# Kernel optimization log

Measured on AMD Instinct MI355X. Metric: run time of the kernel, lower is better.

Reference implementation:

```python
import jax, jax.numpy as jnp
import numpy as np

VOCAB, HIDDEN, NUM_LABELS = 400000, 300, 7
B, S = 256, 512


def setup_inputs() -> dict:
    key = jax.random.key(0)
    ks = jax.random.split(key, 8)
    return {
        "input_ids": jax.random.randint(ks[0], (B, S), 0, VOCAB, dtype=jnp.int64 if jax.config.jax_enable_x64 else jnp.int32).astype(jnp.int32),
        "attention_masks": jax.random.randint(ks[1], (B, S), 0, 2).astype(jnp.int32),
        "labels": jax.random.randint(ks[2], (B,), 0, NUM_LABELS).astype(jnp.int32),
        "drop_mask": jax.random.randint(ks[3], (B, S), 0, 2).astype(jnp.int32),
        "emb_table": jax.random.normal(ks[4], (VOCAB, HIDDEN), dtype=jnp.float32) * 0.1,
        "W1": jax.random.normal(ks[5], (HIDDEN, HIDDEN), dtype=jnp.float32) * 0.05,
        "b1": jnp.zeros((HIDDEN,), jnp.float32),
        "W2": jax.random.normal(ks[6], (HIDDEN, HIDDEN), dtype=jnp.float32) * 0.05,
        "b2": jnp.zeros((HIDDEN,), jnp.float32),
        "W3": jax.random.normal(ks[7], (NUM_LABELS, HIDDEN), dtype=jnp.float32) * 0.05,
        "b3": jnp.zeros((NUM_LABELS,), jnp.float32),
    }


def reference(input_ids, attention_masks, labels, drop_mask, emb_table, W1, b1, W2, b2, W3, b3):
    # masked token ids (padding -> id 0), then embedding gather: [B,S,H]
    masked = input_ids * attention_masks
    embs = emb_table[masked]
    # NOTE: original's per-element torch.mul loop discards results, so the
    # dropout mask only affects the divisor via count_nonzero per row.
    nonzeros = jnp.sum(drop_mask, axis=1).astype(jnp.float32)  # [B]
    avg = jnp.sum(embs, axis=1) / nonzeros[:, None]            # [B,H]
    h = jax.nn.relu(avg @ W1.T + b1)
    h = jax.nn.relu(h @ W2.T + b2)
    logits = h @ W3.T + b3                                     # [B,7]
    logp = jax.nn.log_softmax(logits, axis=-1)
    loss = -jnp.mean(jnp.take_along_axis(logp, labels[:, None], axis=1))
    return loss, logits
```

## Files before the change

kernel.cpp:

```cpp
#include <hip/hip_runtime.h>
#include <hip/hip_bf16.h>

#define B_ 256
#define S_ 512
#define H_ 300
#define NL_ 7
#define NT_ 320
#define NCHUNK_ 4
#define SPER_ (S_ / NCHUNK_)

__global__ __launch_bounds__(NT_) void dan_gather(
    const int* __restrict__ ids, const int* __restrict__ am,
    const float* __restrict__ emb, float* __restrict__ partial) {
  const int b = blockIdx.x, c = blockIdx.y, t = threadIdx.x;
  __shared__ int sid[SPER_];
  const int s0 = c * SPER_;
  for (int s = t; s < SPER_; s += NT_) {
    int off = b * S_ + s0 + s;
    sid[s] = ids[off] * am[off];
  }
  __syncthreads();
  if (t < H_) {
    const float* ep = emb + t;
    float a0 = 0.f, a1 = 0.f, a2 = 0.f, a3 = 0.f;
#pragma unroll 4
    for (int s = 0; s < SPER_; s += 4) {
      int i0 = sid[s], i1 = sid[s + 1], i2 = sid[s + 2], i3 = sid[s + 3];
      a0 += ep[(size_t)i0 * H_];
      a1 += ep[(size_t)i1 * H_];
      a2 += ep[(size_t)i2 * H_];
      a3 += ep[(size_t)i3 * H_];
    }
    partial[(b * NCHUNK_ + c) * H_ + t] = (a0 + a1) + (a2 + a3);
  }
}

__global__ __launch_bounds__(NT_) void dan_mlp(
    const float* __restrict__ partial, const int* __restrict__ drop,
    const int* __restrict__ labels,
    const float* __restrict__ W1, const float* __restrict__ b1,
    const float* __restrict__ W2, const float* __restrict__ b2,
    const float* __restrict__ W3, const float* __restrict__ b3,
    float* __restrict__ out, float* __restrict__ perloss) {
  const int b = blockIdx.x, t = threadIdx.x;
  __shared__ float savg[H_];
  __shared__ float sh[H_];
  __shared__ float swred[NT_ / 64];
  __shared__ float snz;
  __shared__ float slog[NL_];

  int nzp = 0;
  for (int s = t; s < S_; s += NT_) nzp += drop[b * S_ + s];
  for (int o = 32; o > 0; o >>= 1) nzp += __shfl_down(nzp, o, 64);
  if ((t & 63) == 0) swred[t >> 6] = (float)nzp;
  __syncthreads();
  if (t == 0) {
    float s = 0.f;
    for (int w = 0; w < NT_ / 64; ++w) s += swred[w];
    snz = s;
  }
  __syncthreads();

  if (t < H_) {
    float s = 0.f;
#pragma unroll
    for (int c = 0; c < NCHUNK_; ++c) s += partial[(b * NCHUNK_ + c) * H_ + t];
    savg[t] = s / snz;
  }
  __syncthreads();

  if (t < H_) {
    float acc = b1[t];
    const float* w = W1 + t * H_;
    for (int j = 0; j < H_; ++j) acc = fmaf(w[j], savg[j], acc);
    sh[t] = fmaxf(acc, 0.f);
  }
  __syncthreads();

  if (t < H_) {
    float acc = b2[t];
    const float* w = W2 + t * H_;
    for (int j = 0; j < H_; ++j) acc = fmaf(w[j], sh[j], acc);
    savg[t] = fmaxf(acc, 0.f);
  }
  __syncthreads();

  if (t < NL_) {
    float acc = b3[t];
    const float* w = W3 + t * H_;
    for (int j = 0; j < H_; ++j) acc = fmaf(w[j], savg[j], acc);
    slog[t] = acc;
    out[1 + b * NL_ + t] = acc;
  }
  __syncthreads();

  if (t == 0) {
    float m = slog[0];
    for (int c = 1; c < NL_; ++c) m = fmaxf(m, slog[c]);
    float se = 0.f;
    for (int c = 0; c < NL_; ++c) se += expf(slog[c] - m);
    int lab = labels[b];
    perloss[b] = slog[lab] - m - logf(se);
  }
}

__global__ void dan_loss(const float* __restrict__ perloss,
                         float* __restrict__ out) {
  const int t = threadIdx.x;
  float v = perloss[t];
  for (int o = 32; o > 0; o >>= 1) v += __shfl_down(v, o, 64);
  __shared__ float r[4];
  if ((t & 63) == 0) r[t >> 6] = v;
  __syncthreads();
  if (t == 0) out[0] = -(r[0] + r[1] + r[2] + r[3]) * (1.0f / B_);
}

extern "C" void kernel_launch(void* const* d_in, const int* in_sizes, int n_in,
                              void* d_out, int out_size, void* d_ws,
                              size_t ws_size, hipStream_t stream) {
  const int* ids = (const int*)d_in[0];
  const int* am = (const int*)d_in[1];
  const int* labels = (const int*)d_in[2];
  const int* drop = (const int*)d_in[3];
  const float* emb = (const float*)d_in[4];
  const float* W1 = (const float*)d_in[5];
  const float* b1 = (const float*)d_in[6];
  const float* W2 = (const float*)d_in[7];
  const float* b2 = (const float*)d_in[8];
  const float* W3 = (const float*)d_in[9];
  const float* b3 = (const float*)d_in[10];
  float* out = (float*)d_out;

  float* partial = (float*)d_ws;
  float* perloss = partial + (size_t)B_ * NCHUNK_ * H_;

  dan_gather<<<dim3(B_, NCHUNK_), NT_, 0, stream>>>(ids, am, emb, partial);
  dan_mlp<<<B_, NT_, 0, stream>>>(partial, drop, labels, W1, b1, W2, b2, W3,
                                  b3, out, perloss);
  dan_loss<<<1, B_, 0, stream>>>(perloss, out);
}
```

Measured before the change: 46.43 us.

## Compact nonzero token ids before gather and pre-transpose MLP weights

The gather kernel now compacts the nonzero masked ids with a ballot and popcount, so padded tokens (id 0) are not gathered individually. It adds a single (count of padded tokens) * emb[0] term per column to keep the sum exact. The same launch also runs extra blocks that transpose W1 and W2 into workspace, so the MLP's per-thread dot products read weights coalesced across threads instead of striding by row. The cost is extra workspace, extra shared-memory bookkeeping, and a small reordering of float sums.

```diff
diff --git a/kernel.cpp b/kernel.cpp
--- a/kernel.cpp
+++ b/kernel.cpp
@@ -9,37 +9,86 @@
 #define NCHUNK_ 4
 #define SPER_ (S_ / NCHUNK_)
 
-__global__ __launch_bounds__(NT_) void dan_gather(
+#define NGATHER_ (B_ * NCHUNK_)
+#define NTILE_ 10
+#define NTRANS_ (2 * NTILE_ * NTILE_)
+
+__global__ __launch_bounds__(NT_) void dan_gather_t(
     const int* __restrict__ ids, const int* __restrict__ am,
-    const float* __restrict__ emb, float* __restrict__ partial) {
-  const int b = blockIdx.x, c = blockIdx.y, t = threadIdx.x;
-  __shared__ int sid[SPER_];
-  const int s0 = c * SPER_;
-  for (int s = t; s < SPER_; s += NT_) {
-    int off = b * S_ + s0 + s;
-    sid[s] = ids[off] * am[off];
-  }
-  __syncthreads();
-  if (t < H_) {
-    const float* ep = emb + t;
-    float a0 = 0.f, a1 = 0.f, a2 = 0.f, a3 = 0.f;
-#pragma unroll 4
-    for (int s = 0; s < SPER_; s += 4) {
-      int i0 = sid[s], i1 = sid[s + 1], i2 = sid[s + 2], i3 = sid[s + 3];
-      a0 += ep[(size_t)i0 * H_];
-      a1 += ep[(size_t)i1 * H_];
-      a2 += ep[(size_t)i2 * H_];
-      a3 += ep[(size_t)i3 * H_];
+    const float* __restrict__ emb,
+    const float* __restrict__ W1, const float* __restrict__ W2,
+    float* __restrict__ partial, float* __restrict__ WT1,
+    float* __restrict__ WT2) {
+  const int bid = blockIdx.x;
+  const int t = threadIdx.x;
+
+  if (bid < NGATHER_) {
+    const int b = bid >> 2, c = bid & 3;
+    __shared__ int cid[SPER_ + 8];
+    __shared__ int wcnt[2];
+    __shared__ int snnzp;
+
+    int id = 0;
+    if (t < SPER_) {
+      int off = b * S_ + c * SPER_ + t;
+      id = ids[off] * am[off];
     }
-    partial[(b * NCHUNK_ + c) * H_ + t] = (a0 + a1) + (a2 + a3);
+    for (int s = t; s < SPER_ + 8; s += NT_) cid[s] = 0;
+    unsigned long long m = __ballot(id != 0);
+    const int lane = t & 63;
+    if (t < SPER_ && lane == 0) wcnt[t >> 6] = __popcll(m);
+    __syncthreads();
+    if (t < SPER_ && id != 0) {
+      int base = (t >> 6) ? wcnt[0] : 0;
+      int rank = __popcll(m & ((1ull << lane) - 1));
+      cid[base + rank] = id;
+    }
+    if (t == 0) snnzp = (wcnt[0] + wcnt[1] + 7) & ~7;
+    __syncthreads();
+
+    if (t < H_) {
+      const float* ep = emb + t;
+      const int nnzp = snnzp;
+      float a0 = 0.f, a1 = 0.f, a2 = 0.f, a3 = 0.f;
+#pragma unroll 2
+      for (int s = 0; s < nnzp; s += 8) {
+        a0 += ep[(size_t)cid[s] * H_];
+        a1 += ep[(size_t)cid[s + 1] * H_];
+        a2 += ep[(size_t)cid[s + 2] * H_];
+        a3 += ep[(size_t)cid[s + 3] * H_];
+        a0 += ep[(size_t)cid[s + 4] * H_];
+        a1 += ep[(size_t)cid[s + 5] * H_];
+        a2 += ep[(size_t)cid[s + 6] * H_];
+        a3 += ep[(size_t)cid[s + 7] * H_];
+      }
+      float r = (a0 + a1) + (a2 + a3) + (float)(SPER_ - nnzp) * ep[0];
+      partial[bid * H_ + t] = r;
+    }
+  } else {
+    int tid = bid - NGATHER_;
+    const float* src = (tid < NTILE_ * NTILE_) ? W1 : W2;
+    float* dst = (tid < NTILE_ * NTILE_) ? WT1 : WT2;
+    int tile = (tid < NTILE_ * NTILE_) ? tid : tid - NTILE_ * NTILE_;
+    int by = (tile / NTILE_) * 32, bx = (tile % NTILE_) * 32;
+    __shared__ float stile[32][33];
+    int tx = t & 31, ty = t >> 5;
+    for (int r = ty; r < 32; r += 10) {
+      int row = by + r, col = bx + tx;
+      if (row < H_ && col < H_) stile[r][tx] = src[row * H_ + col];
+    }
+    __syncthreads();
+    for (int r = ty; r < 32; r += 10) {
+      int row = bx + r, col = by + tx;
+      if (row < H_ && col < H_) dst[row * H_ + col] = stile[tx][r];
+    }
   }
 }
 
 __global__ __launch_bounds__(NT_) void dan_mlp(
     const float* __restrict__ partial, const int* __restrict__ drop,
     const int* __restrict__ labels,
-    const float* __restrict__ W1, const float* __restrict__ b1,
-    const float* __restrict__ W2, const float* __restrict__ b2,
+    const float* __restrict__ WT1, const float* __restrict__ b1,
+    const float* __restrict__ WT2, const float* __restrict__ b2,
     const float* __restrict__ W3, const float* __restrict__ b3,
     float* __restrict__ out, float* __restrict__ perloss) {
   const int b = blockIdx.x, t = threadIdx.x;
@@ -71,16 +120,18 @@
 
   if (t < H_) {
     float acc = b1[t];
-    const float* w = W1 + t * H_;
-    for (int j = 0; j < H_; ++j) acc = fmaf(w[j], savg[j], acc);
+    const float* w = WT1 + t;
+#pragma unroll 10
+    for (int j = 0; j < H_; ++j) acc = fmaf(w[(size_t)j * H_], savg[j], acc);
     sh[t] = fmaxf(acc, 0.f);
   }
   __syncthreads();
 
   if (t < H_) {
     float acc = b2[t];
-    const float* w = W2 + t * H_;
-    for (int j = 0; j < H_; ++j) acc = fmaf(w[j], sh[j], acc);
+    const float* w = WT2 + t;
+#pragma unroll 10
+    for (int j = 0; j < H_; ++j) acc = fmaf(w[(size_t)j * H_], sh[j], acc);
     savg[t] = fmaxf(acc, 0.f);
   }
   __syncthreads();
@@ -132,10 +183,13 @@
   float* out = (float*)d_out;
 
   float* partial = (float*)d_ws;
-  float* perloss = partial + (size_t)B_ * NCHUNK_ * H_;
+  float* perloss = partial + (size_t)NGATHER_ * H_;
+  float* WT1 = perloss + B_;
+  float* WT2 = WT1 + (size_t)H_ * H_;
 
-  dan_gather<<<dim3(B_, NCHUNK_), NT_, 0, stream>>>(ids, am, emb, partial);
-  dan_mlp<<<B_, NT_, 0, stream>>>(partial, drop, labels, W1, b1, W2, b2, W3,
+  dan_gather_t<<<NGATHER_ + NTRANS_, NT_, 0, stream>>>(ids, am, emb, W1, W2,
+                                                       partial, WT1, WT2);
+  dan_mlp<<<B_, NT_, 0, stream>>>(partial, drop, labels, WT1, b1, WT2, b2, W3,
                                   b3, out, perloss);
   dan_loss<<<1, B_, 0, stream>>>(perloss, out);
 }
```

Result: slower. 50.77 us (+9.3%).

## Fuse gather, MLP and loss into one kernel with last-block reduction

Applied to the files above, without the earlier changes.

Merges the three kernels into a single 640-thread block per batch row. Two thread groups split the sequence for the embedding gather, and the dense layers become wave-per-row dot products with shuffle reductions. The final loss mean is computed by the last block to finish, detected with an atomic counter that is cleared by a memset. This removes two launches and the global partial-sum round trip, but the gather now uses only 256 blocks instead of 1024, which lowers the memory-level parallelism available to it.

```diff
diff --git a/kernel.cpp b/kernel.cpp
--- a/kernel.cpp
+++ b/kernel.cpp
@@ -5,92 +5,108 @@
 #define S_ 512
 #define H_ 300
 #define NL_ 7
-#define NT_ 320
-#define NCHUNK_ 4
-#define SPER_ (S_ / NCHUNK_)
+#define NT_ 640
+#define GRP_ 320
+#define NWAVE_ 10
 
-__global__ __launch_bounds__(NT_) void dan_gather(
+__global__ __launch_bounds__(NT_) void dan_fused(
     const int* __restrict__ ids, const int* __restrict__ am,
-    const float* __restrict__ emb, float* __restrict__ partial) {
-  const int b = blockIdx.x, c = blockIdx.y, t = threadIdx.x;
-  __shared__ int sid[SPER_];
-  const int s0 = c * SPER_;
-  for (int s = t; s < SPER_; s += NT_) {
-    int off = b * S_ + s0 + s;
-    sid[s] = ids[off] * am[off];
-  }
-  __syncthreads();
-  if (t < H_) {
-    const float* ep = emb + t;
-    float a0 = 0.f, a1 = 0.f, a2 = 0.f, a3 = 0.f;
-#pragma unroll 4
-    for (int s = 0; s < SPER_; s += 4) {
-      int i0 = sid[s], i1 = sid[s + 1], i2 = sid[s + 2], i3 = sid[s + 3];
-      a0 += ep[(size_t)i0 * H_];
-      a1 += ep[(size_t)i1 * H_];
-      a2 += ep[(size_t)i2 * H_];
-      a3 += ep[(size_t)i3 * H_];
-    }
-    partial[(b * NCHUNK_ + c) * H_ + t] = (a0 + a1) + (a2 + a3);
-  }
-}
-
-__global__ __launch_bounds__(NT_) void dan_mlp(
-    const float* __restrict__ partial, const int* __restrict__ drop,
-    const int* __restrict__ labels,
+    const int* __restrict__ labels, const int* __restrict__ drop,
+    const float* __restrict__ emb,
     const float* __restrict__ W1, const float* __restrict__ b1,
     const float* __restrict__ W2, const float* __restrict__ b2,
     const float* __restrict__ W3, const float* __restrict__ b3,
-    float* __restrict__ out, float* __restrict__ perloss) {
+    float* __restrict__ out, float* __restrict__ perloss,
+    unsigned* __restrict__ cnt) {
   const int b = blockIdx.x, t = threadIdx.x;
+  __shared__ int sid[S_];
+  __shared__ float sred[H_];
   __shared__ float savg[H_];
-  __shared__ float sh[H_];
-  __shared__ float swred[NT_ / 64];
+  __shared__ float sh1[H_];
+  __shared__ float sh2[H_];
+  __shared__ float swred[8];
   __shared__ float snz;
   __shared__ float slog[NL_];
 
-  int nzp = 0;
-  for (int s = t; s < S_; s += NT_) nzp += drop[b * S_ + s];
-  for (int o = 32; o > 0; o >>= 1) nzp += __shfl_down(nzp, o, 64);
-  if ((t & 63) == 0) swred[t >> 6] = (float)nzp;
+  if (t < S_) {
+    int off = b * S_ + t;
+    sid[t] = ids[off] * am[off];
+    int dv = drop[off];
+    for (int o = 32; o > 0; o >>= 1) dv += __shfl_down(dv, o, 64);
+    if ((t & 63) == 0) swred[t >> 6] = (float)dv;
+  }
   __syncthreads();
   if (t == 0) {
-    float s = 0.f;
-    for (int w = 0; w < NT_ / 64; ++w) s += swred[w];
-    snz = s;
+    float s2 = 0.f;
+    for (int w = 0; w < 8; ++w) s2 += swred[w];
+    snz = s2;
   }
   __syncthreads();
 
-  if (t < H_) {
-    float s = 0.f;
-#pragma unroll
-    for (int c = 0; c < NCHUNK_; ++c) s += partial[(b * NCHUNK_ + c) * H_ + t];
-    savg[t] = s / snz;
+  const int g = (t >= GRP_) ? 1 : 0;
+  const int lt = t - g * GRP_;
+  float a0 = 0.f, a1 = 0.f, a2 = 0.f, a3 = 0.f;
+  if (lt < H_) {
+    const float* ep = emb + lt;
+    const int s0 = g * (S_ / 2);
+#pragma unroll 2
+    for (int s = s0; s < s0 + S_ / 2; s += 8) {
+      a0 += ep[sid[s] * H_];
+      a1 += ep[sid[s + 1] * H_];
+      a2 += ep[sid[s + 2] * H_];
+      a3 += ep[sid[s + 3] * H_];
+      a0 += ep[sid[s + 4] * H_];
+      a1 += ep[sid[s + 5] * H_];
+      a2 += ep[sid[s + 6] * H_];
+      a3 += ep[sid[s + 7] * H_];
+    }
+  }
+  if (g == 1 && lt < H_) sred[lt] = (a0 + a1) + (a2 + a3);
+  __syncthreads();
+  if (g == 0 && lt < H_)
+    savg[lt] = ((a0 + a1) + (a2 + a3) + sred[lt]) / snz;
+  __syncthreads();
+
+  const int wv = t >> 6;
+  const int lane = t & 63;
+
+  for (int i = wv; i < H_; i += NWAVE_) {
+    const float* row = W1 + i * H_;
+    float d = row[lane] * savg[lane];
+    d = fmaf(row[lane + 64], savg[lane + 64], d);
+    d = fmaf(row[lane + 128], savg[lane + 128], d);
+    d = fmaf(row[lane + 192], savg[lane + 192], d);
+    if (lane < H_ - 256) d = fmaf(row[lane + 256], savg[lane + 256], d);
+    for (int o = 32; o > 0; o >>= 1) d += __shfl_xor(d, o, 64);
+    if (lane == 0) sh1[i] = fmaxf(d + b1[i], 0.f);
   }
   __syncthreads();
 
-  if (t < H_) {
-    float acc = b1[t];
-    const float* w = W1 + t * H_;
-    for (int j = 0; j < H_; ++j) acc = fmaf(w[j], savg[j], acc);
-    sh[t] = fmaxf(acc, 0.f);
+  for (int i = wv; i < H_; i += NWAVE_) {
+    const float* row = W2 + i * H_;
+    float d = row[lane] * sh1[lane];
+    d = fmaf(row[lane + 64], sh1[lane + 64], d);
+    d = fmaf(row[lane + 128], sh1[lane + 128], d);
+    d = fmaf(row[lane + 192], sh1[lane + 192], d);
+    if (lane < H_ - 256) d = fmaf(row[lane + 256], sh1[lane + 256], d);
+    for (int o = 32; o > 0; o >>= 1) d += __shfl_xor(d, o, 64);
+    if (lane == 0) sh2[i] = fmaxf(d + b2[i], 0.f);
   }
   __syncthreads();
 
-  if (t < H_) {
-    float acc = b2[t];
-    const float* w = W2 + t * H_;
-    for (int j = 0; j < H_; ++j) acc = fmaf(w[j], sh[j], acc);
-    savg[t] = fmaxf(acc, 0.f);
-  }
-  __syncthreads();
-
-  if (t < NL_) {
-    float acc = b3[t];
-    const float* w = W3 + t * H_;
-    for (int j = 0; j < H_; ++j) acc = fmaf(w[j], savg[j], acc);
-    slog[t] = acc;
-    out[1 + b * NL_ + t] = acc;
+  if (wv < NL_) {
+    const float* row = W3 + wv * H_;
+    float d = row[lane] * sh2[lane];
+    d = fmaf(row[lane + 64], sh2[lane + 64], d);
+    d = fmaf(row[lane + 128], sh2[lane + 128], d);
+    d = fmaf(row[lane + 192], sh2[lane + 192], d);
+    if (lane < H_ - 256) d = fmaf(row[lane + 256], sh2[lane + 256], d);
+    for (int o = 32; o > 0; o >>= 1) d += __shfl_xor(d, o, 64);
+    if (lane == 0) {
+      d += b3[wv];
+      slog[wv] = d;
+      out[1 + b * NL_ + wv] = d;
+    }
   }
   __syncthreads();
 
@@ -102,17 +118,23 @@
     int lab = labels[b];
     perloss[b] = slog[lab] - m - logf(se);
   }
-}
+  __syncthreads();
 
-__global__ void dan_loss(const float* __restrict__ perloss,
-                         float* __restrict__ out) {
-  const int t = threadIdx.x;
-  float v = perloss[t];
-  for (int o = 32; o > 0; o >>= 1) v += __shfl_down(v, o, 64);
-  __shared__ float r[4];
-  if ((t & 63) == 0) r[t >> 6] = v;
-  __syncthreads();
-  if (t == 0) out[0] = -(r[0] + r[1] + r[2] + r[3]) * (1.0f / B_);
+  if (t < 64) {
+    unsigned old = 0;
+    if (t == 0) {
+      __threadfence();
+      old = atomicAdd(cnt, 1u);
+    }
+    old = __shfl(old, 0, 64);
+    if (old == B_ - 1) {
+      __threadfence();
+      float v = perloss[t] + perloss[t + 64] + perloss[t + 128] +
+                perloss[t + 192];
+      for (int o = 32; o > 0; o >>= 1) v += __shfl_xor(v, o, 64);
+      if (t == 0) out[0] = -v * (1.0f / (float)B_);
+    }
+  }
 }
 
 extern "C" void kernel_launch(void* const* d_in, const int* in_sizes, int n_in,
@@ -131,11 +153,10 @@
   const float* b3 = (const float*)d_in[10];
   float* out = (float*)d_out;
 
-  float* partial = (float*)d_ws;
-  float* perloss = partial + (size_t)B_ * NCHUNK_ * H_;
+  float* perloss = (float*)d_ws;
+  unsigned* cnt = (unsigned*)((char*)d_ws + B_ * sizeof(float));
 
-  dan_gather<<<dim3(B_, NCHUNK_), NT_, 0, stream>>>(ids, am, emb, partial);
-  dan_mlp<<<B_, NT_, 0, stream>>>(partial, drop, labels, W1, b1, W2, b2, W3,
-                                  b3, out, perloss);
-  dan_loss<<<1, B_, 0, stream>>>(perloss, out);
+  hipMemsetAsync(cnt, 0, sizeof(unsigned), stream);
+  dan_fused<<<B_, NT_, 0, stream>>>(ids, am, labels, drop, emb, W1, b1, W2,
+                                    b2, W3, b3, out, perloss, cnt);
 }
```

After: 74.84 us. 1.61x slower.

## Vectorize embedding gather with float4 rows split across token groups

Applied to the files above, without the earlier changes.

The gather kernel now has each thread load float4 slices of an embedding row, and the 300 threads are split into four token groups of 75 threads each. The four group partial sums are combined through shared memory. The MLP matvecs also switch to float4 loads of the weights and activations. The aim is fewer, wider memory transactions per gathered row, at the cost of an extra shared-memory reduction and barrier, and strided float4 weight reads per thread.

```diff
diff --git a/kernel.cpp b/kernel.cpp
--- a/kernel.cpp
+++ b/kernel.cpp
@@ -8,31 +8,49 @@
 #define NT_ 320
 #define NCHUNK_ 4
 #define SPER_ (S_ / NCHUNK_)
+#define NGATHER_ (B_ * NCHUNK_)
+
+#define Q_ (H_ / 4)
+
+__device__ __forceinline__ void f4add(float4& a, const float4 b) {
+  a.x += b.x; a.y += b.y; a.z += b.z; a.w += b.w;
+}
 
 __global__ __launch_bounds__(NT_) void dan_gather(
     const int* __restrict__ ids, const int* __restrict__ am,
     const float* __restrict__ emb, float* __restrict__ partial) {
-  const int b = blockIdx.x, c = blockIdx.y, t = threadIdx.x;
+  const int gb = blockIdx.x;
+  const int b = gb >> 2, c = gb & 3;
+  const int t = threadIdx.x;
   __shared__ int sid[SPER_];
-  const int s0 = c * SPER_;
-  for (int s = t; s < SPER_; s += NT_) {
-    int off = b * S_ + s0 + s;
-    sid[s] = ids[off] * am[off];
+  __shared__ __align__(16) float sacc[4][H_];
+
+  if (t < SPER_) {
+    int off = b * S_ + c * SPER_ + t;
+    sid[t] = ids[off] * am[off];
   }
   __syncthreads();
+
   if (t < H_) {
-    const float* ep = emb + t;
-    float a0 = 0.f, a1 = 0.f, a2 = 0.f, a3 = 0.f;
-#pragma unroll 4
-    for (int s = 0; s < SPER_; s += 4) {
-      int i0 = sid[s], i1 = sid[s + 1], i2 = sid[s + 2], i3 = sid[s + 3];
-      a0 += ep[(size_t)i0 * H_];
-      a1 += ep[(size_t)i1 * H_];
-      a2 += ep[(size_t)i2 * H_];
-      a3 += ep[(size_t)i3 * H_];
+    const int grp = t / Q_;
+    const int dq = t - grp * Q_;
+    const float* ebase = emb + 4 * dq;
+    float4 a0 = {0.f, 0.f, 0.f, 0.f}, a1 = {0.f, 0.f, 0.f, 0.f};
+#pragma unroll 8
+    for (int it = 0; it < SPER_ / 4; ++it) {
+      int id = sid[4 * it + grp];
+      const float4 v =
+          *reinterpret_cast<const float4*>(ebase + (size_t)id * H_);
+      if (it & 1) f4add(a1, v); else f4add(a0, v);
     }
-    partial[(b * NCHUNK_ + c) * H_ + t] = (a0 + a1) + (a2 + a3);
+    f4add(a0, a1);
+    *reinterpret_cast<float4*>(&sacc[grp][4 * dq]) = a0;
   }
+  __syncthreads();
+
+  if (t < H_)
+    partial[gb * H_ + t] =
+        (sacc[0][t] + sacc[1][t]) + (sacc[2][t] + sacc[3][t]);
 }
 
 __global__ __launch_bounds__(NT_) void dan_mlp(
@@ -43,8 +61,8 @@
     const float* __restrict__ W3, const float* __restrict__ b3,
     float* __restrict__ out, float* __restrict__ perloss) {
   const int b = blockIdx.x, t = threadIdx.x;
-  __shared__ float savg[H_];
-  __shared__ float sh[H_];
+  __shared__ __align__(16) float savg[H_];
+  __shared__ __align__(16) float sh[H_];
   __shared__ float swred[NT_ / 64];
   __shared__ float snz;
   __shared__ float slog[NL_];
@@ -70,25 +88,50 @@
   __syncthreads();
 
   if (t < H_) {
-    float acc = b1[t];
-    const float* w = W1 + t * H_;
-    for (int j = 0; j < H_; ++j) acc = fmaf(w[j], savg[j], acc);
-    sh[t] = fmaxf(acc, 0.f);
+    const float4* w = reinterpret_cast<const float4*>(W1 + (size_t)t * H_);
+    const float4* x = reinterpret_cast<const float4*>(savg);
+    float4 a = {0.f, 0.f, 0.f, 0.f};
+#pragma unroll 5
+    for (int j = 0; j < Q_; ++j) {
+      float4 wv = w[j], xv = x[j];
+      a.x = fmaf(wv.x, xv.x, a.x);
+      a.y = fmaf(wv.y, xv.y, a.y);
+      a.z = fmaf(wv.z, xv.z, a.z);
+      a.w = fmaf(wv.w, xv.w, a.w);
+    }
+    sh[t] = fmaxf(b1[t] + (a.x + a.y) + (a.z + a.w), 0.f);
   }
   __syncthreads();
 
   if (t < H_) {
-    float acc = b2[t];
-    const float* w = W2 + t * H_;
-    for (int j = 0; j < H_; ++j) acc = fmaf(w[j], sh[j], acc);
-    savg[t] = fmaxf(acc, 0.f);
+    const float4* w = reinterpret_cast<const float4*>(W2 + (size_t)t * H_);
+    const float4* x = reinterpret_cast<const float4*>(sh);
+    float4 a = {0.f, 0.f, 0.f, 0.f};
+#pragma unroll 5
+    for (int j = 0; j < Q_; ++j) {
+      float4 wv = w[j], xv = x[j];
+      a.x = fmaf(wv.x, xv.x, a.x);
+      a.y = fmaf(wv.y, xv.y, a.y);
+      a.z = fmaf(wv.z, xv.z, a.z);
+      a.w = fmaf(wv.w, xv.w, a.w);
+    }
+    savg[t] = fmaxf(b2[t] + (a.x + a.y) + (a.z + a.w), 0.f);
   }
   __syncthreads();
 
   if (t < NL_) {
-    float acc = b3[t];
-    const float* w = W3 + t * H_;
-    for (int j = 0; j < H_; ++j) acc = fmaf(w[j], savg[j], acc);
+    const float4* w = reinterpret_cast<const float4*>(W3 + (size_t)t * H_);
+    const float4* x = reinterpret_cast<const float4*>(savg);
+    float4 a = {0.f, 0.f, 0.f, 0.f};
+#pragma unroll 5
+    for (int j = 0; j < Q_; ++j) {
+      float4 wv = w[j], xv = x[j];
+      a.x = fmaf(wv.x, xv.x, a.x);
+      a.y = fmaf(wv.y, xv.y, a.y);
+      a.z = fmaf(wv.z, xv.z, a.z);
+      a.w = fmaf(wv.w, xv.w, a.w);
+    }
+    float acc = b3[t] + (a.x + a.y) + (a.z + a.w);
     slog[t] = acc;
     out[1 + b * NL_ + t] = acc;
   }
@@ -132,9 +175,9 @@
   float* out = (float*)d_out;
 
   float* partial = (float*)d_ws;
-  float* perloss = partial + (size_t)B_ * NCHUNK_ * H_;
+  float* perloss = partial + (size_t)NGATHER_ * H_;
 
-  dan_gather<<<dim3(B_, NCHUNK_), NT_, 0, stream>>>(ids, am, emb, partial);
+  dan_gather<<<NGATHER_, NT_, 0, stream>>>(ids, am, emb, partial);
   dan_mlp<<<B_, NT_, 0, stream>>>(partial, drop, labels, W1, b1, W2, b2, W3,
                                   b3, out, perloss);
   dan_loss<<<1, B_, 0, stream>>>(perloss, out);
```

New measurement: 46.71 us. Within noise of the previous version (+0.6%).
